# Kernel optimization log

Measured on AMD Instinct MI355X. Metric: run time of the kernel, lower is better.

Reference implementation:

```python
import jax, jax.numpy as jnp
import numpy as np

NUM_USER = 1_000_000
NUM_ITEM = 100_000
LATENT_DIM = 64
NUM_PARTITIONS = 4
NUM_CENTROIDS = 256
CLUSTER_DIM = LATENT_DIM // NUM_PARTITIONS  # 16
BATCH = 4096
N_NEG = 200


def setup_inputs() -> dict:
    key = jax.random.key(0)
    ks = jax.random.split(key, 7)
    user_id = jax.random.randint(ks[0], (BATCH,), 0, NUM_USER)
    pos_id = jax.random.randint(ks[1], (BATCH, 1), 0, NUM_ITEM)
    neg_ids = jax.random.randint(ks[2], (BATCH, N_NEG), 0, NUM_ITEM)
    # learned parameters
    user_table = jax.random.normal(ks[3], (NUM_USER, LATENT_DIM), jnp.float32) * 0.1
    centroids = jax.random.normal(ks[4], (NUM_PARTITIONS, NUM_CENTROIDS, CLUSTER_DIM), jnp.float32) * 0.1
    item_table = jax.random.normal(ks[5], (NUM_ITEM, LATENT_DIM), jnp.float32) * 0.1
    # pre-sampled uniform noise for the gumbel-softmax (one per partition/user/centroid)
    eps = 1e-10
    gumbel_u = jnp.clip(jax.random.uniform(ks[6], (NUM_PARTITIONS, BATCH, NUM_CENTROIDS), jnp.float32), eps, 1.0 - eps)
    return {
        "user_id": user_id,
        "pos_id": pos_id,
        "neg_ids": neg_ids,
        "user_table": user_table,
        "centroids": centroids,
        "item_table": item_table,
        "gumbel_u": gumbel_u,
    }


def _encode_user(user_emb, centroids, gumbel_u):
    # user_emb: [B, D]; centroids: [P, K, C]; gumbel_u: [P, B, K]
    B = user_emb.shape[0]
    P, K, C = centroids.shape
    ue = user_emb.reshape(B, P, C)  # split latent dim into P partitions
    # squared euclidean distance per partition: [B, P, K]
    dist = ((ue ** 2).sum(-1)[..., None]
            + (centroids ** 2).sum(-1)[None, :, :]
            - 2.0 * jnp.einsum('bpc,pkc->bpk', ue, centroids))
    neg_dist = -dist  # logits fed to softmax / gumbel-softmax
    logits = jax.nn.softmax(neg_dist, axis=-1)  # [B, P, K] (self.logits, transposed)
    # gumbel-softmax, tau=1, hard=True (straight-through)
    gumbels = -jnp.log(-jnp.log(gumbel_u))  # [P, B, K]
    y_soft = jax.nn.softmax(neg_dist + jnp.transpose(gumbels, (1, 0, 2)), axis=-1)
    y_hard = jax.nn.one_hot(jnp.argmax(y_soft, axis=-1), K, dtype=y_soft.dtype)
    idx_center = y_hard + y_soft - jax.lax.stop_gradient(y_soft)  # [B, P, K]
    encode = jnp.einsum('bpk,pkc->bpc', idx_center, centroids).reshape(B, P * C)  # [B, D]
    return encode, logits


def reference(user_id, pos_id, neg_ids, user_table, centroids, item_table, gumbel_u):
    user_emb = user_table[user_id]                       # [B, D] gather
    user_vec, _logits = _encode_user(user_emb, centroids, gumbel_u)
    user_vecs = user_vec[:, None, :]                     # [B, 1, D]
    pos_items = item_table[pos_id]                       # [B, 1, D]
    neg_items = item_table[neg_ids]                      # [B, N, D]
    pos_scores = (user_vecs * pos_items).sum(-1)         # [B, 1]
    neg_scores = (user_vecs * neg_items).sum(-1)         # [B, N]
    return (pos_scores, neg_scores)
```

## Files before the change

kernel.cpp:

```cpp
#include <hip/hip_runtime.h>

#define BATCH 4096
#define NNEG  200
#define NITEM 201
#define DIM   64
#define NPART 4
#define NCENT 256
#define CDIM  16
#define CPAD  17
#define USERS_PER_BLOCK 16

__global__ __launch_bounds__(256) void qvae_encode_kernel(
    const int*   __restrict__ user_id,
    const float* __restrict__ user_table,
    const float* __restrict__ centroids,
    const float* __restrict__ gumbel_u,
    float*       __restrict__ user_vec)
{
    __shared__ float cent[NCENT * CPAD];

    const int p    = blockIdx.y;
    const int tid  = threadIdx.x;
    const int w    = tid >> 6;
    const int lane = tid & 63;

    const float* cp = centroids + (size_t)p * NCENT * CDIM;
    for (int idx = tid; idx < NCENT * CDIM; idx += 256) {
        int row = idx >> 4, col = idx & 15;
        cent[row * CPAD + col] = cp[idx];
    }
    __syncthreads();
    {
        float s = 0.f;
        #pragma unroll
        for (int c = 0; c < CDIM; ++c) { float v = cent[tid * CPAD + c]; s += v * v; }
        cent[tid * CPAD + CDIM] = s;
    }
    __syncthreads();

    for (int it = 0; it < USERS_PER_BLOCK / 4; ++it) {
        const int b = blockIdx.x * USERS_PER_BLOCK + it * 4 + w;

        const int uid = user_id[b];
        const float* up = user_table + (size_t)uid * DIM + p * CDIM;
        float ue[CDIM];
        #pragma unroll
        for (int i = 0; i < 4; ++i) {
            float4 v = ((const float4*)up)[i];
            ue[4*i+0] = v.x; ue[4*i+1] = v.y; ue[4*i+2] = v.z; ue[4*i+3] = v.w;
        }
        float ue2 = 0.f;
        #pragma unroll
        for (int c = 0; c < CDIM; ++c) ue2 += ue[c] * ue[c];

        const float* gp = gumbel_u + ((size_t)p * BATCH + b) * NCENT;
        float best_s = -INFINITY;
        int   best_k = 0;
        #pragma unroll
        for (int j = 0; j < 4; ++j) {
            const int k = j * 64 + lane;
            float u = gp[k];
            float g = -logf(-logf(u));
            float dot = 0.f, c2 = cent[k * CPAD + CDIM];
            #pragma unroll
            for (int c = 0; c < CDIM; ++c) dot += ue[c] * cent[k * CPAD + c];
            float dist = (ue2 + c2) - 2.0f * dot;
            float s = -dist + g;
            if (s > best_s) { best_s = s; best_k = k; }
        }

        #pragma unroll
        for (int m = 1; m < 64; m <<= 1) {
            float so = __shfl_xor(best_s, m, 64);
            int   ko = __shfl_xor(best_k, m, 64);
            if (so > best_s || (so == best_s && ko < best_k)) { best_s = so; best_k = ko; }
        }

        if (lane < CDIM) {
            user_vec[(size_t)b * DIM + p * CDIM + lane] = cent[best_k * CPAD + lane];
        }
    }
}

__global__ __launch_bounds__(256) void qvae_score_kernel(
    const int*   __restrict__ pos_id,
    const int*   __restrict__ neg_ids,
    const float* __restrict__ item_table,
    const float* __restrict__ user_vec,
    float*       __restrict__ out)
{
    __shared__ float4 uv4[DIM / 4];
    __shared__ int    ids[NITEM];
    __shared__ float  res[NITEM];

    const int b   = blockIdx.x;
    const int tid = threadIdx.x;

    if (tid < DIM / 4) uv4[tid] = ((const float4*)(user_vec + (size_t)b * DIM))[tid];
    if (tid == 0)           ids[0]   = pos_id[b];
    else if (tid <= NNEG)   ids[tid] = neg_ids[(size_t)b * NNEG + tid - 1];
    __syncthreads();

    const int grp = tid >> 4;
    const int l16 = tid & 15;
    const float4 u = uv4[l16];

    for (int item = grp; item < NITEM; item += 16) {
        const float4 v = ((const float4*)(item_table + (size_t)ids[item] * DIM))[l16];
        float s = v.x * u.x + v.y * u.y + v.z * u.z + v.w * u.w;
        s += __shfl_xor(s, 1, 64);
        s += __shfl_xor(s, 2, 64);
        s += __shfl_xor(s, 4, 64);
        s += __shfl_xor(s, 8, 64);
        if (l16 == 0) res[item] = s;
    }
    __syncthreads();

    if (tid == 0)   out[b] = res[0];
    if (tid < NNEG) out[BATCH + (size_t)b * NNEG + tid] = res[tid + 1];
}

extern "C" void kernel_launch(void* const* d_in, const int* in_sizes, int n_in,
                              void* d_out, int out_size, void* d_ws, size_t ws_size,
                              hipStream_t stream) {
    const int*   user_id    = (const int*)  d_in[0];
    const int*   pos_id     = (const int*)  d_in[1];
    const int*   neg_ids    = (const int*)  d_in[2];
    const float* user_table = (const float*)d_in[3];
    const float* centroids  = (const float*)d_in[4];
    const float* item_table = (const float*)d_in[5];
    const float* gumbel_u   = (const float*)d_in[6];
    float* out = (float*)d_out;
    float* uv  = (float*)d_ws;

    qvae_encode_kernel<<<dim3(BATCH / USERS_PER_BLOCK, NPART), 256, 0, stream>>>(
        user_id, user_table, centroids, gumbel_u, uv);
    qvae_score_kernel<<<BATCH, 256, 0, stream>>>(
        pos_id, neg_ids, item_table, uv, out);
}
```

Before: 351.2 us.

## Swizzle centroid LDS layout for float4 reads and unroll score gathers by two

Stores centroids in shared memory as XOR-swizzled float4 rows with norms kept in a separate array, so the distance loop reads centroids with 128-bit LDS loads instead of padded scalar loads. The score kernel now issues two independent item-row gathers per iteration to raise memory-level parallelism, and gets an occupancy hint in its launch bounds. The user-vector intermediate moves from the workspace to a device global array. The score kernel is bound by random item-table gathers, so these changes may have limited effect; the global array also makes the launch non-reentrant across concurrent calls.

```diff
diff --git a/kernel.cpp b/kernel.cpp
--- a/kernel.cpp
+++ b/kernel.cpp
@@ -7,34 +7,41 @@
 #define NPART 4
 #define NCENT 256
 #define CDIM  16
-#define CPAD  17
 #define USERS_PER_BLOCK 16
+
+__device__ float g_uv[BATCH * DIM];
 
 __global__ __launch_bounds__(256) void qvae_encode_kernel(
     const int*   __restrict__ user_id,
     const float* __restrict__ user_table,
     const float* __restrict__ centroids,
-    const float* __restrict__ gumbel_u,
-    float*       __restrict__ user_vec)
+    const float* __restrict__ gumbel_u)
 {
-    __shared__ float cent[NCENT * CPAD];
+    __shared__ float cent[NCENT * CDIM];
+    __shared__ float cnorm[NCENT];
 
     const int p    = blockIdx.y;
     const int tid  = threadIdx.x;
     const int w    = tid >> 6;
     const int lane = tid & 63;
 
-    const float* cp = centroids + (size_t)p * NCENT * CDIM;
-    for (int idx = tid; idx < NCENT * CDIM; idx += 256) {
-        int row = idx >> 4, col = idx & 15;
-        cent[row * CPAD + col] = cp[idx];
+    const float4* cp4 = (const float4*)(centroids + (size_t)p * NCENT * CDIM);
+    #pragma unroll
+    for (int q = tid; q < NCENT * 4; q += 256) {
+        const int row = q >> 2, f = q & 3;
+        ((float4*)cent)[(row << 2) + (f ^ ((row >> 1) & 3))] = cp4[q];
     }
     __syncthreads();
+
     {
+        const float4* c4 = (const float4*)cent;
         float s = 0.f;
         #pragma unroll
-        for (int c = 0; c < CDIM; ++c) { float v = cent[tid * CPAD + c]; s += v * v; }
-        cent[tid * CPAD + CDIM] = s;
+        for (int f = 0; f < 4; ++f) {
+            const float4 v = c4[(tid << 2) + (f ^ ((tid >> 1) & 3))];
+            s += v.x * v.x + v.y * v.y + v.z * v.z + v.w * v.w;
+        }
+        cnorm[tid] = s;
     }
     __syncthreads();
 
@@ -43,50 +50,57 @@
 
         const int uid = user_id[b];
         const float* up = user_table + (size_t)uid * DIM + p * CDIM;
-        float ue[CDIM];
+        float4 ue4[4];
         #pragma unroll
-        for (int i = 0; i < 4; ++i) {
-            float4 v = ((const float4*)up)[i];
-            ue[4*i+0] = v.x; ue[4*i+1] = v.y; ue[4*i+2] = v.z; ue[4*i+3] = v.w;
-        }
+        for (int i = 0; i < 4; ++i) ue4[i] = ((const float4*)up)[i];
         float ue2 = 0.f;
         #pragma unroll
-        for (int c = 0; c < CDIM; ++c) ue2 += ue[c] * ue[c];
+        for (int i = 0; i < 4; ++i)
+            ue2 += ue4[i].x * ue4[i].x + ue4[i].y * ue4[i].y
+                 + ue4[i].z * ue4[i].z + ue4[i].w * ue4[i].w;
 
         const float* gp = gumbel_u + ((size_t)p * BATCH + b) * NCENT;
+        const float4* c4 = (const float4*)cent;
         float best_s = -INFINITY;
         int   best_k = 0;
         #pragma unroll
         for (int j = 0; j < 4; ++j) {
             const int k = j * 64 + lane;
-            float u = gp[k];
-            float g = -logf(-logf(u));
-            float dot = 0.f, c2 = cent[k * CPAD + CDIM];
+            const float u = gp[k];
+            const float g = -logf(-logf(u));
+            const float c2 = cnorm[k];
+            float dot = 0.f;
             #pragma unroll
-            for (int c = 0; c < CDIM; ++c) dot += ue[c] * cent[k * CPAD + c];
-            float dist = (ue2 + c2) - 2.0f * dot;
-            float s = -dist + g;
+            for (int f = 0; f < 4; ++f) {
+                const float4 v = c4[(k << 2) + (f ^ ((k >> 1) & 3))];
+                dot += ue4[f].x * v.x + ue4[f].y * v.y
+                     + ue4[f].z * v.z + ue4[f].w * v.w;
+            }
+            const float dist = (ue2 + c2) - 2.0f * dot;
+            const float s = -dist + g;
             if (s > best_s) { best_s = s; best_k = k; }
         }
 
         #pragma unroll
         for (int m = 1; m < 64; m <<= 1) {
-            float so = __shfl_xor(best_s, m, 64);
-            int   ko = __shfl_xor(best_k, m, 64);
+            const float so = __shfl_xor(best_s, m, 64);
+            const int   ko = __shfl_xor(best_k, m, 64);
             if (so > best_s || (so == best_s && ko < best_k)) { best_s = so; best_k = ko; }
         }
 
         if (lane < CDIM) {
-            user_vec[(size_t)b * DIM + p * CDIM + lane] = cent[best_k * CPAD + lane];
+            const int f = lane >> 2;
+            const int slot = f ^ ((best_k >> 1) & 3);
+            g_uv[(size_t)b * DIM + p * CDIM + lane] =
+                cent[(best_k << 4) + (slot << 2) + (lane & 3)];
         }
     }
 }
 
-__global__ __launch_bounds__(256) void qvae_score_kernel(
+__global__ __launch_bounds__(256, 8) void qvae_score_kernel(
     const int*   __restrict__ pos_id,
     const int*   __restrict__ neg_ids,
     const float* __restrict__ item_table,
-    const float* __restrict__ user_vec,
     float*       __restrict__ out)
 {
     __shared__ float4 uv4[DIM / 4];
@@ -96,7 +110,7 @@
     const int b   = blockIdx.x;
     const int tid = threadIdx.x;
 
-    if (tid < DIM / 4) uv4[tid] = ((const float4*)(user_vec + (size_t)b * DIM))[tid];
+    if (tid < DIM / 4) uv4[tid] = ((const float4*)(g_uv + (size_t)b * DIM))[tid];
     if (tid == 0)           ids[0]   = pos_id[b];
     else if (tid <= NNEG)   ids[tid] = neg_ids[(size_t)b * NNEG + tid - 1];
     __syncthreads();
@@ -105,14 +119,29 @@
     const int l16 = tid & 15;
     const float4 u = uv4[l16];
 
-    for (int item = grp; item < NITEM; item += 16) {
-        const float4 v = ((const float4*)(item_table + (size_t)ids[item] * DIM))[l16];
-        float s = v.x * u.x + v.y * u.y + v.z * u.z + v.w * u.w;
-        s += __shfl_xor(s, 1, 64);
-        s += __shfl_xor(s, 2, 64);
-        s += __shfl_xor(s, 4, 64);
-        s += __shfl_xor(s, 8, 64);
-        if (l16 == 0) res[item] = s;
+    for (int item = grp; item < NITEM; item += 32) {
+        const int itemB = item + 16;
+        const bool hasB = (itemB < NITEM);
+
+        const float4 v1 = ((const float4*)(item_table + (size_t)ids[item] * DIM))[l16];
+        float4 v2;
+        if (hasB) v2 = ((const float4*)(item_table + (size_t)ids[itemB] * DIM))[l16];
+
+        float s1 = v1.x * u.x + v1.y * u.y + v1.z * u.z + v1.w * u.w;
+        s1 += __shfl_xor(s1, 1, 64);
+        s1 += __shfl_xor(s1, 2, 64);
+        s1 += __shfl_xor(s1, 4, 64);
+        s1 += __shfl_xor(s1, 8, 64);
+        if (l16 == 0) res[item] = s1;
+
+        if (hasB) {
+            float s2 = v2.x * u.x + v2.y * u.y + v2.z * u.z + v2.w * u.w;
+            s2 += __shfl_xor(s2, 1, 64);
+            s2 += __shfl_xor(s2, 2, 64);
+            s2 += __shfl_xor(s2, 4, 64);
+            s2 += __shfl_xor(s2, 8, 64);
+            if (l16 == 0) res[itemB] = s2;
+        }
     }
     __syncthreads();
 
@@ -131,10 +160,10 @@
     const float* item_table = (const float*)d_in[5];
     const float* gumbel_u   = (const float*)d_in[6];
     float* out = (float*)d_out;
-    float* uv  = (float*)d_ws;
+    (void)d_ws; (void)ws_size;
 
     qvae_encode_kernel<<<dim3(BATCH / USERS_PER_BLOCK, NPART), 256, 0, stream>>>(
-        user_id, user_table, centroids, gumbel_u, uv);
+        user_id, user_table, centroids, gumbel_u);
     qvae_score_kernel<<<BATCH, 256, 0, stream>>>(
-        pos_id, neg_ids, item_table, uv, out);
+        pos_id, neg_ids, item_table, out);
 }
```

Result: no change. 349.3 us (-0.5%).
